# Kernel tuning notes

Hardware: AMD Instinct MI355X
Metric: run time of the kernel (lower is better)

The kernel has to match this reference:

```python
import jax, jax.numpy as jnp
import numpy as np

K = 16
SIGMA_ONE = 0.02
EXP_RANGE = 10.0
T_MIN = 1e-6


def setup_inputs() -> dict:
    key = jax.random.key(0)
    ks = jax.random.split(key, 6)
    B, D, H = 32, 49152, 16
    return {
        "mu": jax.random.normal(ks[0], (B, D), dtype=jnp.float32),
        "t": jax.random.uniform(ks[1], (B, 1), dtype=jnp.float32),
        "W1": jax.random.normal(ks[2], (2, H), dtype=jnp.float32) * 0.5,
        "b1": jax.random.normal(ks[3], (H,), dtype=jnp.float32) * 0.1,
        "W2": jax.random.normal(ks[4], (H, 2), dtype=jnp.float32) * 0.1,
        "b2": jax.random.normal(ks[5], (2,), dtype=jnp.float32) * 0.1,
    }


def reference(mu, t, W1, b1, W2, b2):
    # bin geometry: centers (2K-1)/K - 1 for K=1..k, lower/upper = center -/+ 1/k
    k_idx = jnp.arange(1, K + 1, dtype=mu.dtype)
    k_centers = (2.0 * k_idx - 1.0) / K - 1.0          # [K]
    k_lower = k_centers - 1.0 / K
    k_upper = k_centers + 1.0 / K

    gamma = 1.0 - jnp.power(jnp.asarray(SIGMA_ONE, mu.dtype), 2.0 * t)  # [B,1]

    # inner model: pointwise MLP on stacked (mu, t) -> (mean_eps, log_var_eps)
    x = jnp.stack([mu, jnp.broadcast_to(t, mu.shape)], axis=-1)  # [B,D,2]
    h = jax.nn.gelu(x @ W1 + b1)                                 # [B,D,H]
    out = h @ W2 + b2                                            # [B,D,2]
    mu_eps, ln_sigma_eps = out[..., 0], out[..., 1]

    var_scale = jnp.sqrt((1.0 - gamma) / gamma)                  # [B,1]
    mu_x = mu / gamma - var_scale * mu_eps                       # [B,D]
    sigma_x = jnp.maximum(
        var_scale * jnp.exp(jnp.clip(ln_sigma_eps, -EXP_RANGE, EXP_RANGE)),
        SIGMA_ONE,
    )
    cond = t < T_MIN                                             # [B,1]
    mu_x = jnp.where(cond, 0.0, mu_x)
    sigma_x = jnp.where(cond, 1.0, sigma_x)

    inv = (1.0 / (sigma_x * jnp.sqrt(jnp.asarray(2.0, mu.dtype))))[..., None]  # [B,D,1]
    mu_b = mu_x[..., None]                                       # [B,D,1]

    def normal_cdf(bins):  # bins [K] -> [B,D,K]
        return 0.5 * (1.0 + jax.lax.erf((bins - mu_b) * inv))

    cdf_lower = jnp.where(k_lower <= -1.0, 0.0, normal_cdf(k_lower))
    cdf_upper = jnp.where(k_upper >= 1.0, 1.0, normal_cdf(k_upper))
    return cdf_upper - cdf_lower                                 # [B,D,K]
```

## Files before the change

kernel.cpp:

```cpp
#include <hip/hip_runtime.h>
#include <math.h>

#define KBINS 16
#define HID 16
#define LN_SIGMA1 (-3.912023005428146f)

__device__ __forceinline__ float to_sgpr(float x) {
    return __int_as_float(__builtin_amdgcn_readfirstlane(__float_as_int(x)));
}

__global__ __launch_bounds__(256, 4) void bfn_kernel(
    const float* __restrict__ mu,
    const float* __restrict__ t,
    const float* __restrict__ W1,
    const float* __restrict__ b1,
    const float* __restrict__ W2,
    const float* __restrict__ b2,
    float* __restrict__ out,
    int D)
{
    __shared__ float lds[256 * 20];

    const int b   = blockIdx.y;
    const int tid = threadIdx.x;
    const int d0  = blockIdx.x * 256;
    const int d   = d0 + tid;
    const bool valid = (d < D);

    const float tb    = t[b];
    const float gamma = -expm1f(2.0f * tb * LN_SIGMA1);
    const float e2t   = 1.0f - gamma;
    const float inv_gamma = 1.0f / gamma;
    const float var_scale = sqrtf(e2t * inv_gamma);
    const bool  tiny_t = (tb < 1e-6f);

    float w1a[HID], c1[HID], w20[HID], w21[HID];
#pragma unroll
    for (int i = 0; i < HID; ++i) {
        w1a[i] = to_sgpr(W1[i]);
        c1[i]  = fmaf(tb, W1[HID + i], b1[i]);
        w20[i] = to_sgpr(W2[2 * i]);
        w21[i] = to_sgpr(W2[2 * i + 1]);
    }
    const float bias0 = to_sgpr(b2[0]);
    const float bias1 = to_sgpr(b2[1]);

    const float m = valid ? mu[(size_t)b * D + d] : 0.0f;

    float o0 = bias0, o1 = bias1;
#pragma unroll
    for (int i = 0; i < HID; ++i) {
        float pre = fmaf(m, w1a[i], c1[i]);
        float p2  = pre * pre;
        float z   = pre * fmaf(p2, -0.0713552235f, -1.5957691216f);
        float e   = __expf(z);
        float h   = pre * __builtin_amdgcn_rcpf(1.0f + e);
        o0 = fmaf(h, w20[i], o0);
        o1 = fmaf(h, w21[i], o1);
    }

    float mu_x = fmaf(m, inv_gamma, -var_scale * o0);
    float lse  = fminf(fmaxf(o1, -10.0f), 10.0f);
    float sigma_x = fmaxf(var_scale * __expf(lse), 0.02f);
    if (tiny_t) { mu_x = 0.0f; sigma_x = 1.0f; }

    const float inv = 0.70710678118f * __builtin_amdgcn_rcpf(sigma_x);
    const float x0  = (-0.875f - mu_x) * inv;
    const float stp = 0.125f * inv;

    float cdf[KBINS + 1];
    cdf[0] = 0.0f; cdf[KBINS] = 1.0f;
#pragma unroll
    for (int j = 1; j < KBINS; ++j) {
        float x  = fmaf((float)(j - 1), stp, x0);
        float ax = fabsf(x);
        float p  = fmaf(0.078108f, ax, 0.000972f);
        p        = fmaf(p, ax, 0.230389f);
        p        = fmaf(p, ax, 0.278393f);
        float q  = fmaf(p, ax, 1.0f);
        float q2 = q * q;
        float q4 = q2 * q2;
        float hr = 0.5f * __builtin_amdgcn_rcpf(q4);
        cdf[j] = (x >= 0.0f) ? (1.0f - hr) : hr;
    }

    const bool full = (d0 + 256 <= D);
    if (full) {
        float4* row = (float4*)(lds + tid * 20);
#pragma unroll
        for (int s = 0; s < 4; ++s)
            row[s] = make_float4(cdf[4*s+1] - cdf[4*s],   cdf[4*s+2] - cdf[4*s+1],
                                 cdf[4*s+3] - cdf[4*s+2], cdf[4*s+4] - cdf[4*s+3]);
        __syncthreads();
        float4* og = (float4*)out + ((size_t)b * D + d0) * 4;
#pragma unroll
        for (int s = 0; s < 4; ++s) {
            int f = s * 256 + tid;
            int e = f >> 2;
            int c = (f & 3) << 2;
            og[f] = *(const float4*)(lds + e * 20 + c);
        }
    } else if (valid) {
        float4* op = (float4*)(out + ((size_t)b * D + d) * (size_t)KBINS);
#pragma unroll
        for (int s = 0; s < 4; ++s)
            op[s] = make_float4(cdf[4*s+1] - cdf[4*s],   cdf[4*s+2] - cdf[4*s+1],
                                 cdf[4*s+3] - cdf[4*s+2], cdf[4*s+4] - cdf[4*s+3]);
    }
}

extern "C" void kernel_launch(void* const* d_in, const int* in_sizes, int n_in,
                              void* d_out, int out_size, void* d_ws, size_t ws_size,
                              hipStream_t stream) {
    const float* mu = (const float*)d_in[0];
    const float* t  = (const float*)d_in[1];
    const float* W1 = (const float*)d_in[2];
    const float* b1 = (const float*)d_in[3];
    const float* W2 = (const float*)d_in[4];
    const float* b2 = (const float*)d_in[5];
    float* out = (float*)d_out;

    const int B = in_sizes[1];
    const int D = in_sizes[0] / B;

    dim3 block(256);
    dim3 grid((D + 255) / 256, B);
    bfn_kernel<<<grid, block, 0, stream>>>(mu, t, W1, b1, W2, b2, out, D);
}
```

Measured before the change: 122.1 us.

## Process two elements per thread and use nontemporal stores for output

Each thread now handles two mu elements (512 per block), interleaving their MLP evaluation for more ILP and amortizing the per-block weight setup over twice the work. The output tile in LDS doubles to 512 rows, and global writes switch to nontemporal stores to avoid polluting the cache with the large write-only output. The costs are higher register pressure, a doubled LDS footprint that may reduce occupancy, and half as many blocks in the grid.

```diff
diff --git a/kernel.cpp b/kernel.cpp
--- a/kernel.cpp
+++ b/kernel.cpp
@@ -5,8 +5,54 @@
 #define HID 16
 #define LN_SIGMA1 (-3.912023005428146f)
 
+typedef float floatx4 __attribute__((ext_vector_type(4)));
+
 __device__ __forceinline__ float to_sgpr(float x) {
     return __int_as_float(__builtin_amdgcn_readfirstlane(__float_as_int(x)));
+}
+
+__device__ __forceinline__ void bins16(
+    float m, float o0, float o1,
+    float inv_gamma, float var_scale, bool tiny_t,
+    floatx4 r[4])
+{
+    float mu_x = fmaf(m, inv_gamma, -var_scale * o0);
+    float lse  = fminf(fmaxf(o1, -10.0f), 10.0f);
+    float sigma_x = fmaxf(var_scale * __expf(lse), 0.02f);
+    if (tiny_t) { mu_x = 0.0f; sigma_x = 1.0f; }
+
+    const float inv = 0.70710678118f * __builtin_amdgcn_rcpf(sigma_x);
+    const float x0  = (-0.875f - mu_x) * inv;
+    const float stp = 0.125f * inv;
+
+    float prev = 0.0f;
+#pragma unroll
+    for (int s = 0; s < 4; ++s) {
+        float v[4];
+#pragma unroll
+        for (int q = 0; q < 4; ++q) {
+            const int j = 4 * s + q + 1;
+            float cur;
+            if (j == KBINS) {
+                cur = 1.0f;
+            } else {
+                float x  = fmaf((float)(j - 1), stp, x0);
+                float ax = fabsf(x);
+                float p  = fmaf(0.078108f, ax, 0.000972f);
+                p        = fmaf(p, ax, 0.230389f);
+                p        = fmaf(p, ax, 0.278393f);
+                float qq = fmaf(p, ax, 1.0f);
+                float q2 = qq * qq;
+                float q4 = q2 * q2;
+                float hr = 0.5f * __builtin_amdgcn_rcpf(q4);
+                cur = (x >= 0.0f) ? (1.0f - hr) : hr;
+            }
+            v[q] = cur - prev;
+            prev = cur;
+        }
+        floatx4 rr = { v[0], v[1], v[2], v[3] };
+        r[s] = rr;
+    }
 }
 
 __global__ __launch_bounds__(256, 4) void bfn_kernel(
@@ -19,13 +65,19 @@
     float* __restrict__ out,
     int D)
 {
-    __shared__ float lds[256 * 20];
+    __shared__ float lds[512 * 20];
 
     const int b   = blockIdx.y;
     const int tid = threadIdx.x;
-    const int d0  = blockIdx.x * 256;
-    const int d   = d0 + tid;
-    const bool valid = (d < D);
+    const int d0  = blockIdx.x * 512;
+
+    const int dA = d0 + tid;
+    const int dB = d0 + 256 + tid;
+    const bool vA = (dA < D);
+    const bool vB = (dB < D);
+
+    const float mA = vA ? mu[(size_t)b * D + dA] : 0.0f;
+    const float mB = vB ? mu[(size_t)b * D + dB] : 0.0f;
 
     const float tb    = t[b];
     const float gamma = -expm1f(2.0f * tb * LN_SIGMA1);
@@ -45,67 +97,66 @@
     const float bias0 = to_sgpr(b2[0]);
     const float bias1 = to_sgpr(b2[1]);
 
-    const float m = valid ? mu[(size_t)b * D + d] : 0.0f;
-
-    float o0 = bias0, o1 = bias1;
+    float oA0 = bias0, oA1 = bias1;
+    float oB0 = bias0, oB1 = bias1;
 #pragma unroll
     for (int i = 0; i < HID; ++i) {
-        float pre = fmaf(m, w1a[i], c1[i]);
-        float p2  = pre * pre;
-        float z   = pre * fmaf(p2, -0.0713552235f, -1.5957691216f);
-        float e   = __expf(z);
-        float h   = pre * __builtin_amdgcn_rcpf(1.0f + e);
-        o0 = fmaf(h, w20[i], o0);
-        o1 = fmaf(h, w21[i], o1);
+        float preA = fmaf(mA, w1a[i], c1[i]);
+        float preB = fmaf(mB, w1a[i], c1[i]);
+        float pA2  = preA * preA;
+        float pB2  = preB * preB;
+        float zA   = preA * fmaf(pA2, -0.0713552235f, -1.5957691216f);
+        float zB   = preB * fmaf(pB2, -0.0713552235f, -1.5957691216f);
+        float eA   = __expf(zA);
+        float eB   = __expf(zB);
+        float hA   = preA * __builtin_amdgcn_rcpf(1.0f + eA);
+        float hB   = preB * __builtin_amdgcn_rcpf(1.0f + eB);
+        oA0 = fmaf(hA, w20[i], oA0);
+        oA1 = fmaf(hA, w21[i], oA1);
+        oB0 = fmaf(hB, w20[i], oB0);
+        oB1 = fmaf(hB, w21[i], oB1);
     }
 
-    float mu_x = fmaf(m, inv_gamma, -var_scale * o0);
-    float lse  = fminf(fmaxf(o1, -10.0f), 10.0f);
-    float sigma_x = fmaxf(var_scale * __expf(lse), 0.02f);
-    if (tiny_t) { mu_x = 0.0f; sigma_x = 1.0f; }
-
-    const float inv = 0.70710678118f * __builtin_amdgcn_rcpf(sigma_x);
-    const float x0  = (-0.875f - mu_x) * inv;
-    const float stp = 0.125f * inv;
-
-    float cdf[KBINS + 1];
-    cdf[0] = 0.0f; cdf[KBINS] = 1.0f;
+    const bool full = (d0 + 512 <= D);
+    if (full) {
+        {
+            floatx4 r[4];
+            bins16(mA, oA0, oA1, inv_gamma, var_scale, tiny_t, r);
+            floatx4* rowA = (floatx4*)(lds + tid * 20);
 #pragma unroll
-    for (int j = 1; j < KBINS; ++j) {
-        float x  = fmaf((float)(j - 1), stp, x0);
-        float ax = fabsf(x);
-        float p  = fmaf(0.078108f, ax, 0.000972f);
-        p        = fmaf(p, ax, 0.230389f);
-        p        = fmaf(p, ax, 0.278393f);
-        float q  = fmaf(p, ax, 1.0f);
-        float q2 = q * q;
-        float q4 = q2 * q2;
-        float hr = 0.5f * __builtin_amdgcn_rcpf(q4);
-        cdf[j] = (x >= 0.0f) ? (1.0f - hr) : hr;
-    }
-
-    const bool full = (d0 + 256 <= D);
-    if (full) {
-        float4* row = (float4*)(lds + tid * 20);
+            for (int s = 0; s < 4; ++s) rowA[s] = r[s];
+        }
+        {
+            floatx4 r[4];
+            bins16(mB, oB0, oB1, inv_gamma, var_scale, tiny_t, r);
+            floatx4* rowB = (floatx4*)(lds + (tid + 256) * 20);
 #pragma unroll
-        for (int s = 0; s < 4; ++s)
-            row[s] = make_float4(cdf[4*s+1] - cdf[4*s],   cdf[4*s+2] - cdf[4*s+1],
-                                 cdf[4*s+3] - cdf[4*s+2], cdf[4*s+4] - cdf[4*s+3]);
+            for (int s = 0; s < 4; ++s) rowB[s] = r[s];
+        }
         __syncthreads();
-        float4* og = (float4*)out + ((size_t)b * D + d0) * 4;
+        floatx4* og = (floatx4*)out + ((size_t)b * D + d0) * 4;
 #pragma unroll
-        for (int s = 0; s < 4; ++s) {
+        for (int s = 0; s < 8; ++s) {
             int f = s * 256 + tid;
             int e = f >> 2;
             int c = (f & 3) << 2;
-            og[f] = *(const float4*)(lds + e * 20 + c);
+            __builtin_nontemporal_store(*(const floatx4*)(lds + e * 20 + c), og + f);
         }
-    } else if (valid) {
-        float4* op = (float4*)(out + ((size_t)b * D + d) * (size_t)KBINS);
+    } else {
+        if (vA) {
+            floatx4 r[4];
+            bins16(mA, oA0, oA1, inv_gamma, var_scale, tiny_t, r);
+            floatx4* op = (floatx4*)(out + ((size_t)b * D + dA) * (size_t)KBINS);
 #pragma unroll
-        for (int s = 0; s < 4; ++s)
-            op[s] = make_float4(cdf[4*s+1] - cdf[4*s],   cdf[4*s+2] - cdf[4*s+1],
-                                 cdf[4*s+3] - cdf[4*s+2], cdf[4*s+4] - cdf[4*s+3]);
+            for (int s = 0; s < 4; ++s) op[s] = r[s];
+        }
+        if (vB) {
+            floatx4 r[4];
+            bins16(mB, oB0, oB1, inv_gamma, var_scale, tiny_t, r);
+            floatx4* op = (floatx4*)(out + ((size_t)b * D + dB) * (size_t)KBINS);
+#pragma unroll
+            for (int s = 0; s < 4; ++s) op[s] = r[s];
+        }
     }
 }
 
@@ -124,6 +175,6 @@
     const int D = in_sizes[0] / B;
 
     dim3 block(256);
-    dim3 grid((D + 255) / 256, B);
+    dim3 grid((D + 511) / 512, B);
     bfn_kernel<<<grid, block, 0, stream>>>(mu, t, W1, b1, W2, b2, out, D);
 }
```

Result: slower. 125.6 us (+2.9%).
